# Performance work log

Measured on AMD Instinct MI355X. Metric: run time of the kernel, lower is better.

Reference implementation:

```python
import jax, jax.numpy as jnp
import numpy as np

DT = 0.1
GAMMA_MIN, GAMMA_MAX = 2.0, 3.0
EPS_MIN, EPS_MAX = 0.5, 1.5
B, T, N_INP, N_HID = 64, 1024, 128, 512


def setup_inputs() -> dict:
    key = jax.random.key(0)
    k_x, k_x2h, k_h2h, k_b, k_g, k_e = jax.random.split(key, 6)
    x = jax.random.normal(k_x, (B, T, N_INP), dtype=jnp.float32)
    x2h = jax.random.uniform(k_x2h, (N_INP, N_HID), dtype=jnp.float32)
    # orthogonal init via QR of a random normal matrix
    a = jax.random.normal(k_h2h, (N_HID, N_HID), dtype=jnp.float32)
    q, r = jnp.linalg.qr(a)
    h2h = q * jnp.sign(jnp.diag(r))[None, :]
    bias = jax.random.uniform(k_b, (N_HID,), dtype=jnp.float32) * 2.0 - 1.0
    gamma = jax.random.uniform(k_g, (N_HID,), dtype=jnp.float32) * (GAMMA_MAX - GAMMA_MIN) + GAMMA_MIN
    epsilon = jax.random.uniform(k_e, (N_HID,), dtype=jnp.float32) * (EPS_MAX - EPS_MIN) + EPS_MIN
    return {"x": x, "x2h": x2h, "h2h": h2h, "bias": bias, "gamma": gamma, "epsilon": epsilon}


def reference(x, x2h, h2h, bias, gamma, epsilon):
    Bsz = x.shape[0]
    nh = h2h.shape[0]
    h2h_T = h2h.T

    def step(carry, xt):
        hy, hz = carry  # [B, H] each
        i2h = xt @ x2h                       # [B, H]
        pre = jnp.tanh(hy @ h2h + bias)      # [B, H]
        hz = hz + DT * (jnp.tanh(i2h) - pre @ h2h_T - gamma * hy - epsilon * hz)
        hy = hy + DT * hz
        return (hy, hz), hy

    hy0 = jnp.zeros((Bsz, nh), dtype=x.dtype)
    hz0 = jnp.zeros((Bsz, nh), dtype=x.dtype)
    xs = jnp.swapaxes(x, 0, 1)               # [T, B, I]
    (hy, hz), ys = jax.lax.scan(step, (hy0, hz0), xs)
    all_states = jnp.swapaxes(ys, 0, 1)      # [B, T, H]
    return all_states, hy
```

## Files before the change

kernel.cpp:

```cpp
#include <hip/hip_runtime.h>
#include <stdint.h>

#define Bsz 64
#define Tsz 1024
#define NIc 128
#define NHc 512
#define DTc 0.1f
#define NWG 32
#define JW  16
#define FLG 16

typedef __attribute__((ext_vector_type(8))) short short8;
typedef __attribute__((ext_vector_type(4))) float f32x4;
typedef unsigned long long u64_t;

__device__ __forceinline__ unsigned short f2bf(float f) {
  union { float f; uint32_t u; } v; v.f = f;
  return (unsigned short)((v.u + 0x7fffu + ((v.u >> 16) & 1u)) >> 16);
}
__device__ __forceinline__ float bf2f(unsigned short h) {
  union { float f; uint32_t u; } v; v.u = ((uint32_t)h) << 16; return v.f;
}
__device__ __forceinline__ float fast_tanh(float xx) {
  float a = __builtin_fabsf(xx);
  float e = __expf(-2.0f * a);
  float r = (1.0f - e) / (1.0f + e);
  return __builtin_copysignf(r, xx);
}

__device__ __forceinline__ void wait_flags(int* flags, int target, int tid) {
  if (tid < NWG) {
    while (__hip_atomic_load(&flags[tid * FLG], __ATOMIC_RELAXED,
                             __HIP_MEMORY_SCOPE_AGENT) < target)
      __builtin_amdgcn_s_sleep(1);
  }
  __syncthreads();
  __builtin_amdgcn_fence(__ATOMIC_ACQUIRE, "agent");
}
__device__ __forceinline__ void publish_flag(int* flags, int g, int val, int tid) {
  __builtin_amdgcn_fence(__ATOMIC_RELEASE, "agent");
  __syncthreads();
  if (tid == 0)
    __hip_atomic_store(&flags[g * FLG], val, __ATOMIC_RELAXED,
                       __HIP_MEMORY_SCOPE_AGENT);
}

__device__ __forceinline__ void wait_nf(int* flags, int target, int tid) {
  if (tid < NWG) {
    while (__hip_atomic_load(&flags[tid * FLG], __ATOMIC_RELAXED,
                             __HIP_MEMORY_SCOPE_AGENT) < target)
      __builtin_amdgcn_s_sleep(1);
  }
  __syncthreads();
}
__device__ __forceinline__ void publish_nf(unsigned short* dst ,
                                           const unsigned short* bnc ,
                                           int J0, int* flag_addr, int val, int tid) {
  __syncthreads();
  {
    const u64_t v = ((const u64_t*)bnc)[tid];
    const int row = tid >> 2, q = tid & 3;
    __hip_atomic_store((u64_t*)(dst + row * NHc + J0 + q * 4), v,
                       __ATOMIC_RELAXED, __HIP_MEMORY_SCOPE_AGENT);
  }
  asm volatile("s_waitcnt vmcnt(0)" ::: "memory");
  __syncthreads();
  if (tid == 0)
    __hip_atomic_store(flag_addr, val, __ATOMIC_RELAXED, __HIP_MEMORY_SCOPE_AGENT);
}
__device__ __forceinline__ short8 ld_frag(const u64_t* base64, int idx64) {
  union { u64_t q[2]; short8 s; } u;
  u.q[0] = __hip_atomic_load(base64 + idx64, __ATOMIC_RELAXED, __HIP_MEMORY_SCOPE_AGENT);
  u.q[1] = __hip_atomic_load(base64 + idx64 + 1, __ATOMIC_RELAXED, __HIP_MEMORY_SCOPE_AGENT);
  return u.s;
}

__global__ __launch_bounds__(256, 1)
void pirn_kernel(const float* __restrict__ x, const float* __restrict__ x2h,
                 const float* __restrict__ h2h, const float* __restrict__ bias,
                 const float* __restrict__ gam_p, const float* __restrict__ eps_p,
                 float* __restrict__ out, char* __restrict__ ws)
{
  __shared__ __align__(16) char lds[35328];
  const int g    = blockIdx.x;
  const int tid  = threadIdx.x;
  const int lane = tid & 63;
  const int wv   = tid >> 6;
  const int l15  = lane & 15;
  const int quad = lane >> 4;

  int* hyflag   = (int*)ws;
  int* preflag  = (int*)(ws + 2048);
  int* prolflag = (int*)(ws + 4096);
  unsigned short* hybuf  = (unsigned short*)(ws + 8192);
  unsigned short* prebuf = (unsigned short*)(ws + 8192 + 131072);

  {
    unsigned short* x2ht_hi = (unsigned short*)lds;
    unsigned short* x2ht_lo = (unsigned short*)(lds + 17408);
    const long R0 = (long)g * 2048;
    for (int pass = 0; pass < 8; ++pass) {
      const int c0 = pass * 64;
      __syncthreads();
      for (int i = tid; i < 64 * NIc; i += 256) {
        int c = i & 63; int k = i >> 6;
        float v = x2h[k * NHc + c0 + c];
        unsigned short hi = f2bf(v);
        x2ht_hi[c * 136 + k] = hi;
        x2ht_lo[c * 136 + k] = f2bf(v - bf2f(hi));
      }
      __syncthreads();
      for (int mt = wv * 32; mt < wv * 32 + 32; ++mt) {
        const float* xr = x + (R0 + mt * 16 + l15) * NIc;
        short8 ahi[4], alo[4];
#pragma unroll
        for (int kb = 0; kb < 4; ++kb) {
          int k0 = kb * 32 + quad * 8;
          f32x4 v0 = *(const f32x4*)(xr + k0);
          f32x4 v1 = *(const f32x4*)(xr + k0 + 4);
#pragma unroll
          for (int e = 0; e < 4; ++e) {
            unsigned short h0 = f2bf(v0[e]);
            ahi[kb][e] = (short)h0;
            alo[kb][e] = (short)f2bf(v0[e] - bf2f(h0));
            unsigned short h1 = f2bf(v1[e]);
            ahi[kb][e + 4] = (short)h1;
            alo[kb][e + 4] = (short)f2bf(v1[e] - bf2f(h1));
          }
        }
#pragma unroll
        for (int nt = 0; nt < 4; ++nt) {
          f32x4 acc0 = {0.f, 0.f, 0.f, 0.f};
          f32x4 acc1 = {0.f, 0.f, 0.f, 0.f};
#pragma unroll
          for (int kb = 0; kb < 4; ++kb) {
            int k0 = kb * 32 + quad * 8;
            short8 bhi = *(const short8*)(x2ht_hi + (nt * 16 + l15) * 136 + k0);
            short8 blo = *(const short8*)(x2ht_lo + (nt * 16 + l15) * 136 + k0);
            acc0 = __builtin_amdgcn_mfma_f32_16x16x32_bf16(ahi[kb], bhi, acc0, 0, 0, 0);
            acc1 = __builtin_amdgcn_mfma_f32_16x16x32_bf16(alo[kb], bhi, acc1, 0, 0, 0);
            acc0 = __builtin_amdgcn_mfma_f32_16x16x32_bf16(ahi[kb], blo, acc0, 0, 0, 0);
          }
          long orow = R0 + mt * 16 + quad * 4;
          int oc = c0 + nt * 16 + l15;
#pragma unroll
          for (int r = 0; r < 4; ++r)
            out[(orow + r) * NHc + oc] = fast_tanh(acc0[r] + acc1[r]);
        }
      }
    }
  }
  publish_flag(prolflag, g, 1, tid);

  unsigned short* hcolT = (unsigned short*)lds;
  unsigned short* hrow  = (unsigned short*)(lds + 16640);
  unsigned short* bnc   = (unsigned short*)(lds + 33280);
  const int J0 = g * JW;
  for (int i = tid; i < JW * NHc; i += 256) {
    int jj = i & 15, k = i >> 4;
    hcolT[jj * 520 + k] = f2bf(h2h[k * NHc + J0 + jj]);
  }
  for (int i = tid; i < JW * NHc; i += 256) {
    int k = i & 511, jj = i >> 9;
    hrow[jj * 520 + k] = f2bf(h2h[(J0 + jj) * NHc + k]);
  }
  const int jcol = J0 + l15;
  const float b_c = bias[jcol];
  const float gm  = gam_p[jcol];
  const float ep  = eps_p[jcol];
  __syncthreads();
  wait_flags(prolflag, 1, tid);

  short8 bc[16], br[16];
#pragma unroll
  for (int kb = 0; kb < 16; ++kb) {
    bc[kb] = *(const short8*)(hcolT + l15 * 520 + kb * 32 + quad * 8);
    br[kb] = *(const short8*)(hrow  + l15 * 520 + kb * 32 + quad * 8);
  }

  const int arow = wv * 16 + l15;
  const int brow = wv * 16 + quad * 4;
  const int fbase = arow * NHc;
  float hy_r[4] = {0.f, 0.f, 0.f, 0.f};
  float hz_r[4] = {0.f, 0.f, 0.f, 0.f};
  float pre_r[4];

  for (int t = 0; t < Tsz; ++t) {
    float u_r[4];
#pragma unroll
    for (int r = 0; r < 4; ++r)
      u_r[r] = out[((long)(brow + r) * Tsz + t) * NHc + jcol];

    if (t > 0) {
      wait_nf(hyflag, t, tid);
      const u64_t* hb64 = (const u64_t*)(hybuf + (size_t)(t & 1) * (Bsz * NHc));
      short8 af[16];
#pragma unroll
      for (int kb = 0; kb < 16; ++kb)
        af[kb] = ld_frag(hb64, (fbase + kb * 32 + quad * 8) >> 2);
      f32x4 a0 = {0.f, 0.f, 0.f, 0.f}, a1 = {0.f, 0.f, 0.f, 0.f};
#pragma unroll
      for (int kb = 0; kb < 16; kb += 2) {
        a0 = __builtin_amdgcn_mfma_f32_16x16x32_bf16(af[kb],     bc[kb],     a0, 0, 0, 0);
        a1 = __builtin_amdgcn_mfma_f32_16x16x32_bf16(af[kb + 1], bc[kb + 1], a1, 0, 0, 0);
      }
#pragma unroll
      for (int r = 0; r < 4; ++r) pre_r[r] = fast_tanh(a0[r] + a1[r] + b_c);
    } else {
#pragma unroll
      for (int r = 0; r < 4; ++r) pre_r[r] = fast_tanh(b_c);
    }

    unsigned short* pb = prebuf + (size_t)(t & 1) * (Bsz * NHc);
#pragma unroll
    for (int r = 0; r < 4; ++r)
      bnc[(brow + r) * 16 + l15] = f2bf(pre_r[r]);
    publish_nf(pb, bnc, J0, &preflag[g * FLG], t + 1, tid);
    wait_nf(preflag, t + 1, tid);

    const u64_t* pb64 = (const u64_t*)pb;
    short8 af2[16];
#pragma unroll
    for (int kb = 0; kb < 16; ++kb)
      af2[kb] = ld_frag(pb64, (fbase + kb * 32 + quad * 8) >> 2);
    f32x4 c0v = {0.f, 0.f, 0.f, 0.f}, c1v = {0.f, 0.f, 0.f, 0.f};
#pragma unroll
    for (int kb = 0; kb < 16; kb += 2) {
      c0v = __builtin_amdgcn_mfma_f32_16x16x32_bf16(af2[kb],     br[kb],     c0v, 0, 0, 0);
      c1v = __builtin_amdgcn_mfma_f32_16x16x32_bf16(af2[kb + 1], br[kb + 1], c1v, 0, 0, 0);
    }

#pragma unroll
    for (int r = 0; r < 4; ++r) {
      float c2 = c0v[r] + c1v[r];
      float hz = hz_r[r] + DTc * (u_r[r] - c2 - gm * hy_r[r] - ep * hz_r[r]);
      hz_r[r] = hz;
      hy_r[r] += DTc * hz;
    }

    if (t + 1 < Tsz) {
      unsigned short* hbw = hybuf + (size_t)((t + 1) & 1) * (Bsz * NHc);
#pragma unroll
      for (int r = 0; r < 4; ++r)
        bnc[(brow + r) * 16 + l15] = f2bf(hy_r[r]);
      publish_nf(hbw, bnc, J0, &hyflag[g * FLG], t + 1, tid);
#pragma unroll
      for (int r = 0; r < 4; ++r)
        out[((long)(brow + r) * Tsz + t) * NHc + jcol] = hy_r[r];
    } else {
#pragma unroll
      for (int r = 0; r < 4; ++r)
        out[((long)(brow + r) * Tsz + t) * NHc + jcol] = hy_r[r];
#pragma unroll
      for (int r = 0; r < 4; ++r)
        out[(long)Bsz * Tsz * NHc + (long)(brow + r) * NHc + jcol] = hy_r[r];
    }
  }
}

extern "C" void kernel_launch(void* const* d_in, const int* in_sizes, int n_in,
                              void* d_out, int out_size, void* d_ws, size_t ws_size,
                              hipStream_t stream) {
  const float* x    = (const float*)d_in[0];
  const float* x2h  = (const float*)d_in[1];
  const float* h2h  = (const float*)d_in[2];
  const float* bias = (const float*)d_in[3];
  const float* gam  = (const float*)d_in[4];
  const float* eps  = (const float*)d_in[5];
  (void)in_sizes; (void)n_in; (void)out_size; (void)ws_size;
  pirn_kernel<<<dim3(NWG), dim3(256), 0, stream>>>(
      x, x2h, h2h, bias, gam, eps, (float*)d_out, (char*)d_ws);
}
```

Baseline: 12.31 ms.

## Spread input projection prologue over 256 workgroups and pack sync flags into bytes

The x@x2h+tanh prologue is now split across 256 workgroups instead of 32, so each does an eighth of the rows. Only the first 32 workgroups continue into the recurrence, and they wait on 256 byte-wide prologue flags checked as 64-bit words. Per-step hy/pre flags become wrapping byte epochs packed contiguously, so one wavefront polls all 32 with a single vote instead of strided int flags. This risks flags sharing cache lines, which can add contention, and relies on wraparound epoch comparison.

```diff
diff --git a/kernel.cpp b/kernel.cpp
--- a/kernel.cpp
+++ b/kernel.cpp
@@ -6,9 +6,9 @@
 #define NIc 128
 #define NHc 512
 #define DTc 0.1f
-#define NWG 32
+#define NWGR 32
+#define GRID 256
 #define JW  16
-#define FLG 16
 
 typedef __attribute__((ext_vector_type(8))) short short8;
 typedef __attribute__((ext_vector_type(4))) float f32x4;
@@ -28,34 +28,27 @@
   return __builtin_copysignf(r, xx);
 }
 
-__device__ __forceinline__ void wait_flags(int* flags, int target, int tid) {
-  if (tid < NWG) {
-    while (__hip_atomic_load(&flags[tid * FLG], __ATOMIC_RELAXED,
-                             __HIP_MEMORY_SCOPE_AGENT) < target)
-      __builtin_amdgcn_s_sleep(1);
-  }
-  __syncthreads();
-  __builtin_amdgcn_fence(__ATOMIC_ACQUIRE, "agent");
-}
-__device__ __forceinline__ void publish_flag(int* flags, int g, int val, int tid) {
-  __builtin_amdgcn_fence(__ATOMIC_RELEASE, "agent");
-  __syncthreads();
-  if (tid == 0)
-    __hip_atomic_store(&flags[g * FLG], val, __ATOMIC_RELAXED,
-                       __HIP_MEMORY_SCOPE_AGENT);
-}
-
-__device__ __forceinline__ void wait_nf(int* flags, int target, int tid) {
-  if (tid < NWG) {
-    while (__hip_atomic_load(&flags[tid * FLG], __ATOMIC_RELAXED,
-                             __HIP_MEMORY_SCOPE_AGENT) < target)
-      __builtin_amdgcn_s_sleep(1);
-  }
-  __syncthreads();
-}
-__device__ __forceinline__ void publish_nf(unsigned short* dst ,
-                                           const unsigned short* bnc ,
-                                           int J0, int* flag_addr, int val, int tid) {
+__device__ __forceinline__ void wait_epoch(const unsigned char* flags, int target, int tid) {
+  const int lane = tid & 63;
+  if (tid < 64) {
+    const unsigned char tgt = (unsigned char)target;
+    bool done;
+    do {
+      bool ok = true;
+      if (lane < NWGR) {
+        unsigned char b = __hip_atomic_load(&flags[lane], __ATOMIC_RELAXED,
+                                            __HIP_MEMORY_SCOPE_AGENT);
+        ok = ((unsigned char)(b - tgt) < 128u);
+      }
+      done = __all(ok);
+      if (!done) __builtin_amdgcn_s_sleep(1);
+    } while (!done);
+  }
+  __syncthreads();
+}
+__device__ __forceinline__ void publish_epoch(unsigned short* dst ,
+                                              const unsigned short* bnc ,
+                                              int J0, unsigned char* flag, int epoch, int tid) {
   __syncthreads();
   {
     const u64_t v = ((const u64_t*)bnc)[tid];
@@ -66,7 +59,8 @@
   asm volatile("s_waitcnt vmcnt(0)" ::: "memory");
   __syncthreads();
   if (tid == 0)
-    __hip_atomic_store(flag_addr, val, __ATOMIC_RELAXED, __HIP_MEMORY_SCOPE_AGENT);
+    __hip_atomic_store(flag, (unsigned char)epoch, __ATOMIC_RELAXED,
+                       __HIP_MEMORY_SCOPE_AGENT);
 }
 __device__ __forceinline__ short8 ld_frag(const u64_t* base64, int idx64) {
   union { u64_t q[2]; short8 s; } u;
@@ -89,16 +83,16 @@
   const int l15  = lane & 15;
   const int quad = lane >> 4;
 
-  int* hyflag   = (int*)ws;
-  int* preflag  = (int*)(ws + 2048);
-  int* prolflag = (int*)(ws + 4096);
+  unsigned char* prolflags = (unsigned char*)ws;
+  unsigned char* hyfl      = (unsigned char*)(ws + 1024);
+  unsigned char* prefl     = (unsigned char*)(ws + 1152);
   unsigned short* hybuf  = (unsigned short*)(ws + 8192);
   unsigned short* prebuf = (unsigned short*)(ws + 8192 + 131072);
 
   {
     unsigned short* x2ht_hi = (unsigned short*)lds;
     unsigned short* x2ht_lo = (unsigned short*)(lds + 17408);
-    const long R0 = (long)g * 2048;
+    const long R0 = (long)g * 256;
     for (int pass = 0; pass < 8; ++pass) {
       const int c0 = pass * 64;
       __syncthreads();
@@ -110,7 +104,7 @@
         x2ht_lo[c * 136 + k] = f2bf(v - bf2f(hi));
       }
       __syncthreads();
-      for (int mt = wv * 32; mt < wv * 32 + 32; ++mt) {
+      for (int mt = wv * 4; mt < wv * 4 + 4; ++mt) {
         const float* xr = x + (R0 + mt * 16 + l15) * NIc;
         short8 ahi[4], alo[4];
 #pragma unroll
@@ -150,7 +144,13 @@
       }
     }
   }
-  publish_flag(prolflag, g, 1, tid);
+  __syncthreads();
+  if (tid == 0) {
+    __builtin_amdgcn_fence(__ATOMIC_RELEASE, "agent");
+    __hip_atomic_store(&prolflags[g], (unsigned char)1, __ATOMIC_RELAXED,
+                       __HIP_MEMORY_SCOPE_AGENT);
+  }
+  if (g >= NWGR) return;
 
   unsigned short* hcolT = (unsigned short*)lds;
   unsigned short* hrow  = (unsigned short*)(lds + 16640);
@@ -169,7 +169,24 @@
   const float gm  = gam_p[jcol];
   const float ep  = eps_p[jcol];
   __syncthreads();
-  wait_flags(prolflag, 1, tid);
+  {
+    const u64_t* pf = (const u64_t*)prolflags;
+    if (tid < 64) {
+      bool done;
+      do {
+        bool ok = true;
+        if (lane < 32) {
+          u64_t v = __hip_atomic_load(&pf[lane], __ATOMIC_RELAXED,
+                                      __HIP_MEMORY_SCOPE_AGENT);
+          ok = (v == 0x0101010101010101ull);
+        }
+        done = __all(ok);
+        if (!done) __builtin_amdgcn_s_sleep(8);
+      } while (!done);
+    }
+    __syncthreads();
+    __builtin_amdgcn_fence(__ATOMIC_ACQUIRE, "agent");
+  }
 
   short8 bc[16], br[16];
 #pragma unroll
@@ -192,7 +209,7 @@
       u_r[r] = out[((long)(brow + r) * Tsz + t) * NHc + jcol];
 
     if (t > 0) {
-      wait_nf(hyflag, t, tid);
+      wait_epoch(hyfl, t, tid);
       const u64_t* hb64 = (const u64_t*)(hybuf + (size_t)(t & 1) * (Bsz * NHc));
       short8 af[16];
 #pragma unroll
@@ -215,8 +232,8 @@
 #pragma unroll
     for (int r = 0; r < 4; ++r)
       bnc[(brow + r) * 16 + l15] = f2bf(pre_r[r]);
-    publish_nf(pb, bnc, J0, &preflag[g * FLG], t + 1, tid);
-    wait_nf(preflag, t + 1, tid);
+    publish_epoch(pb, bnc, J0, &prefl[g], t + 1, tid);
+    wait_epoch(prefl, t + 1, tid);
 
     const u64_t* pb64 = (const u64_t*)pb;
     short8 af2[16];
@@ -243,7 +260,7 @@
 #pragma unroll
       for (int r = 0; r < 4; ++r)
         bnc[(brow + r) * 16 + l15] = f2bf(hy_r[r]);
-      publish_nf(hbw, bnc, J0, &hyflag[g * FLG], t + 1, tid);
+      publish_epoch(hbw, bnc, J0, &hyfl[g], t + 1, tid);
 #pragma unroll
       for (int r = 0; r < 4; ++r)
         out[((long)(brow + r) * Tsz + t) * NHc + jcol] = hy_r[r];
@@ -268,6 +285,6 @@
   const float* gam  = (const float*)d_in[4];
   const float* eps  = (const float*)d_in[5];
   (void)in_sizes; (void)n_in; (void)out_size; (void)ws_size;
-  pirn_kernel<<<dim3(NWG), dim3(256), 0, stream>>>(
+  pirn_kernel<<<dim3(GRID), dim3(256), 0, stream>>>(
       x, x2h, h2h, bias, gam, eps, (float*)d_out, (char*)d_ws);
 }
```

Measured after the change: 13.16 ms. 6.9% more time.
